# Optimization experiments

Measured on AMD Instinct MI355X. Metric: run time of the kernel, lower is better.

## Reference

```python
import jax, jax.numpy as jnp
import numpy as np
from jax import lax

B, C, DM, NL, NROI, HID, RHID, REMB = 2, 32, 64, 4, 90, 64, 64, 32
S = DM * DM * DM
EPS = 1e-5
DN = ('NCDHW', 'OIDHW', 'NCDHW')


def setup_inputs() -> dict:
    key = jax.random.key(0)
    ks = jax.random.split(key, 14)
    w = lambda k, shp, s=0.05: (jax.random.normal(k, shp, jnp.float32) * s)
    atlas = (jax.random.uniform(ks[1], (NROI, S)) < 0.1).astype(jnp.float32)
    return {
        'data': jax.random.normal(ks[0], (B, 1, DM, DM, DM), jnp.float32),
        'atlas_mask': atlas,
        'conv0_w': w(ks[2], (C, 1, 3, 3, 3), 0.2),
        'conv0_b': w(ks[3], (C,)),
        'convs_w': w(ks[4], (NL - 1, C, C, 3, 3, 3)),
        'convs_b': w(ks[5], (NL - 1, C)),
        'scale_w1': w(ks[6], (NROI, C, HID)),
        'scale_b1': w(ks[7], (NROI, HID)),
        'scale_w2': w(ks[8], (NROI, HID, C)),
        'scale_b2': w(ks[9], (NROI, C)),
        'proj_w1': w(ks[10], (NROI, C, RHID)),
        'proj_b1': w(ks[11], (NROI, RHID)),
        'proj_w2': w(ks[12], (NROI, RHID, REMB)),
        'proj_b2': w(ks[13], (NROI, REMB)),
    }


def _inorm(x):
    # InstanceNorm3d(affine=False): normalize per (batch, channel) over spatial dims
    m = jnp.mean(x, axis=(2, 3, 4), keepdims=True)
    v = jnp.var(x, axis=(2, 3, 4), keepdims=True)
    return (x - m) * lax.rsqrt(v + EPS)


def _conv(x, w, b):
    y = lax.conv_general_dilated(x, w, (1, 1, 1), 'SAME', dimension_numbers=DN)
    return y + b[None, :, None, None, None]


def reference(data, atlas_mask, conv0_w, conv0_b, convs_w, convs_b,
              scale_w1, scale_b1, scale_w2, scale_b2,
              proj_w1, proj_b1, proj_w2, proj_b2):
    x = jax.nn.relu(_inorm(_conv(data, conv0_w, conv0_b)))
    for i in range(NL - 1):  # fixed small layer loop
        x = jax.nn.relu(_inorm(_conv(x, convs_w[i], convs_b[i])))
    emb = x.reshape(B, C, S)                                  # (B,C,S)
    # (B,C,S) x (S,n_roi) -> (B,n_roi,C), normalized by ROI voxel count
    roi = jnp.einsum('bcs,rs->brc', emb, atlas_mask)
    roi = roi / atlas_mask.sum(axis=-1)[None, :, None]
    # per-ROI gated MLP experts, batched over the roi axis
    h = jax.nn.relu(jnp.einsum('brc,rch->brh', roi, scale_w1) + scale_b1[None])
    gate = jax.nn.sigmoid(jnp.einsum('brh,rhc->brc', h, scale_w2) + scale_b2[None])
    f = gate * roi
    p = jax.nn.relu(jnp.einsum('brc,rch->brh', f, proj_w1) + proj_b1[None])
    out = jnp.einsum('brh,rhe->bre', p, proj_w2) + proj_b2[None]
    return out  # (B, n_roi, roi_emb)
```

## Files before the change

kernel.cpp:

```cpp
#include <hip/hip_runtime.h>
#include <hip/hip_bf16.h>
#include <math.h>

#define S_TOT 262144
#define EPS_F 1e-5f
#define NPART 512
#define PL8   8008

typedef __attribute__((ext_vector_type(8))) short s16x8;
typedef __attribute__((ext_vector_type(4))) float f32x4;
typedef __attribute__((ext_vector_type(4))) unsigned u32x4;

__device__ __forceinline__ unsigned short f2bf(float f) {
    unsigned u = __builtin_bit_cast(unsigned, f);
    unsigned r = (u + 0x7FFFu + ((u >> 16) & 1u)) >> 16;
    return (unsigned short)r;
}
__device__ __forceinline__ float bf2f(unsigned short u) {
    return __builtin_bit_cast(float, ((unsigned)u) << 16);
}
__device__ __forceinline__ unsigned cvt_pk_bf16(float a, float b) {
    unsigned r;
    asm("v_cvt_pk_bf16_f32 %0, %1, %2" : "=v"(r) : "v"(a), "v"(b));
    return r;
}

__global__ __launch_bounds__(256)
void prep_w_k(const float* __restrict__ conv0_w, const float* __restrict__ convs_w,
              unsigned short* __restrict__ wpad, unsigned short* __restrict__ whp)
{
    int idx = blockIdx.x * 256 + threadIdx.x;
    if (idx < 2048) {
        int brow = idx >> 5, k = idx & 31;
        int cout = 2 * (brow & 15) + (brow >> 4);
        float wv = (k < 27) ? conv0_w[cout * 27 + k] : 0.f;
        unsigned short hi = f2bf(wv);
        unsigned short lo = f2bf(wv - bf2f(hi));
        wpad[brow * 32 + k]        = hi;
        wpad[1024 + brow * 32 + k] = lo;
        return;
    }
    int j = idx - 2048;
    if (j >= 3 * 27648) return;
    int layer = j / 27648 + 1;
    int rem   = j % 27648;
    int tap   = rem >> 10;
    int cout  = (rem >> 5) & 31;
    int cin   = rem & 31;
    float wv = convs_w[(((layer - 1) * 32 + cout) * 32 + cin) * 27 + tap];
    unsigned short hi = f2bf(wv);
    int brow = ((cout & 1) << 4) | (cout >> 1);
    whp[(size_t)(layer - 1) * 27648 + tap * 1024 + brow * 32 + cin] = hi;
}

__global__ __launch_bounds__(512, 2)
void conv0_k(const float* __restrict__ in, const unsigned short* __restrict__ w0,
             unsigned short* __restrict__ outb, float* __restrict__ raw_out)
{
    __shared__ unsigned short sc[1824];
    __shared__ float s_red[512];

    const int tid  = threadIdx.x;
    const int lane = tid & 63;
    const int wv   = tid >> 6;
    const int row  = lane & 15;
    const int g4   = lane >> 4;

    const int blk = blockIdx.x;
    const int b   = blk >> 8;
    const int t   = blk & 255;
    const int x0  = (t & 7) << 3;
    const int y0  = ((t >> 3) & 7) << 3;
    const int z0  = (t >> 6) << 4;

    for (int i = tid; i < 1800; i += 512) {
        int zz = i / 100, r2 = i - zz * 100, yy = r2 / 10, xx = r2 - yy * 10;
        int gz = z0 + zz - 1, gy = y0 + yy - 1, gx = x0 + xx - 1;
        float v = 0.f;
        if ((unsigned)gz < 64u && (unsigned)gy < 64u && (unsigned)gx < 64u)
            v = in[((size_t)b << 18) + (gz << 12) + (gy << 6) + gx];
        sc[i] = (unsigned short)cvt_pk_bf16(v, v);
    }
    __syncthreads();

    int dvox[8];
    #pragma unroll
    for (int j = 0; j < 8; ++j) {
        int tap = g4 * 8 + j;
        if (tap < 27) {
            int dz = tap / 9, r9 = tap - dz * 9, dy = r9 / 3, dx = r9 - dy * 3;
            dvox[j] = dz * 100 + dy * 10 + dx;
        } else dvox[j] = 0;
    }

    s16x8 wh0 = *(const s16x8*)(w0 + row * 32 + g4 * 8);
    s16x8 wh1 = *(const s16x8*)(w0 + (16 + row) * 32 + g4 * 8);
    s16x8 wl0 = *(const s16x8*)(w0 + 1024 + row * 32 + g4 * 8);
    s16x8 wl1 = *(const s16x8*)(w0 + 1024 + (16 + row) * 32 + g4 * 8);

    f32x4 acc[2][4][2] = {};
    #pragma unroll
    for (int pl = 0; pl < 2; ++pl) {
        #pragma unroll
        for (int f = 0; f < 4; ++f) {
            int vvx = f * 16 + row;
            int base = (2 * wv + pl) * 100 + (vvx >> 3) * 10 + (vvx & 7);
            s16x8 a;
            #pragma unroll
            for (int j = 0; j < 8; ++j) a[j] = (short)sc[base + dvox[j]];
            acc[pl][f][0] = __builtin_amdgcn_mfma_f32_16x16x32_bf16(a, wh0, acc[pl][f][0], 0, 0, 0);
            acc[pl][f][0] = __builtin_amdgcn_mfma_f32_16x16x32_bf16(a, wl0, acc[pl][f][0], 0, 0, 0);
            acc[pl][f][1] = __builtin_amdgcn_mfma_f32_16x16x32_bf16(a, wh1, acc[pl][f][1], 0, 0, 0);
            acc[pl][f][1] = __builtin_amdgcn_mfma_f32_16x16x32_bf16(a, wl1, acc[pl][f][1], 0, 0, 0);
        }
    }

    {
        float s0 = 0.f, ss0 = 0.f, s1 = 0.f, ss1 = 0.f;
        #pragma unroll
        for (int pl = 0; pl < 2; ++pl)
            #pragma unroll
            for (int f = 0; f < 4; ++f)
                #pragma unroll
                for (int q = 0; q < 4; ++q) {
                    float v0 = acc[pl][f][0][q], v1 = acc[pl][f][1][q];
                    s0 += v0; ss0 += v0 * v0; s1 += v1; ss1 += v1 * v1;
                }
        s0 += __shfl_xor(s0, 16); s0 += __shfl_xor(s0, 32);
        ss0 += __shfl_xor(ss0, 16); ss0 += __shfl_xor(ss0, 32);
        s1 += __shfl_xor(s1, 16); s1 += __shfl_xor(s1, 32);
        ss1 += __shfl_xor(ss1, 16); ss1 += __shfl_xor(ss1, 32);
        if (lane < 16) {
            s_red[(wv * 32 + 2 * row) * 2]         = s0;
            s_red[(wv * 32 + 2 * row) * 2 + 1]     = ss0;
            s_red[(wv * 32 + 2 * row + 1) * 2]     = s1;
            s_red[(wv * 32 + 2 * row + 1) * 2 + 1] = ss1;
        }
    }

    #pragma unroll
    for (int pl = 0; pl < 2; ++pl) {
        int zp = 2 * wv + pl;
        unsigned short* ob = outb
            + ((((size_t)b << 18) + ((size_t)(z0 + zp) << 12) + (y0 << 6) + x0) << 5)
            + (row << 1);
        #pragma unroll
        for (int f = 0; f < 4; ++f) {
            #pragma unroll
            for (int qq = 0; qq < 4; ++qq) {
                int u = g4 * 4 + qq;
                int yy = f * 2 + (u >> 3), xx = u & 7;
                unsigned pk = cvt_pk_bf16(acc[pl][f][0][qq], acc[pl][f][1][qq]);
                *(unsigned*)(ob + ((yy << 6) + xx) * 32) = pk;
            }
        }
    }

    __syncthreads();
    if (tid < 64) {
        int n = tid & 31, sel = tid >> 5;
        float tot = 0.f;
        #pragma unroll
        for (int w = 0; w < 8; ++w) tot += s_red[(w * 32 + n) * 2 + sel];
        atomicAdd(&raw_out[(b * 32 + n) * 2 + sel], tot);
    }
}

__global__ __launch_bounds__(512, 4)
void conv_slab_k(const unsigned short* __restrict__ in, const unsigned short* __restrict__ whp_l,
                 const float* __restrict__ raw_in, unsigned short* __restrict__ outb,
                 float* __restrict__ raw_out)
{
    __shared__ unsigned short tile[4 * PL8];
    __shared__ float s_red[512];

    const int tid  = threadIdx.x;
    const int lane = tid & 63;
    const int wv   = tid >> 6;
    const int row  = lane & 15;
    const int g4   = lane >> 4;
    const int g    = tid & 3;
    const int vox0 = tid >> 2;

    const int blk = blockIdx.x;
    const int b   = blk >> 9;
    const int t   = blk & 511;
    const int x0  = (t & 7) << 3;
    const int y0  = ((t >> 3) & 7) << 3;
    const int z0  = (t >> 6) << 3;

    {
        float rs[8], sh[8];
        #pragma unroll
        for (int j = 0; j < 8; ++j) {
            int c = b * 32 + g * 8 + j;
            float sm = raw_in[c * 2], sq = raw_in[c * 2 + 1];
            float mean = sm * (1.f / 262144.f);
            float var  = sq * (1.f / 262144.f) - mean * mean;
            float r = rsqrtf(var + EPS_F);
            rs[j] = r; sh[j] = -mean * r;
        }
        #pragma unroll 1
        for (int u = 0; u < 8; ++u) {
            int vox = vox0 + u * 128;
            if (vox >= 1000) break;
            int zz = vox / 100, r2 = vox - zz * 100, yy = r2 / 10, xx = r2 - yy * 10;
            int gz = z0 + zz - 1, gy = y0 + yy - 1, gx = x0 + xx - 1;
            u32x4 w = (u32x4)0;
            if ((unsigned)gz < 64u && (unsigned)gy < 64u && (unsigned)gx < 64u) {
                u32x4 rv = *(const u32x4*)(in
                    + ((((size_t)b << 18) + (gz << 12) + (gy << 6) + gx) << 5) + (g << 3));
                #pragma unroll
                for (int k = 0; k < 4; ++k) {
                    float ve = __builtin_bit_cast(float, rv[k] << 16);
                    float vo = __builtin_bit_cast(float, rv[k] & 0xFFFF0000u);
                    float ne = fmaxf(0.f, fmaf(ve, rs[2 * k],     sh[2 * k]));
                    float no = fmaxf(0.f, fmaf(vo, rs[2 * k + 1], sh[2 * k + 1]));
                    w[k] = cvt_pk_bf16(ne, no);
                }
            }
            *(u32x4*)&tile[g * PL8 + (vox << 3)] = w;
        }
    }
    __syncthreads();

    f32x4 acc[4][2] = {};
    {
        const unsigned short* aplane = &tile[g4 * PL8];
        int abase[4];
        #pragma unroll
        for (int f = 0; f < 4; ++f) {
            int vvx = f * 16 + row;
            abase[f] = ((wv * 100 + (vvx >> 3) * 10 + (vvx & 7)) << 3);
        }
        const unsigned short* wrow = whp_l + row * 32 + g4 * 8;

        s16x8 wh0 = *(const s16x8*)(wrow);
        s16x8 wh1 = *(const s16x8*)(wrow + 512);

        #pragma unroll 1
        for (int tap = 0; tap < 27; ++tap) {
            int ntap = (tap < 26) ? tap + 1 : 26;
            const unsigned short* wn = wrow + ntap * 1024;
            s16x8 nh0 = *(const s16x8*)(wn);
            s16x8 nh1 = *(const s16x8*)(wn + 512);

            int dz = tap / 9, r9 = tap - dz * 9, dy = r9 / 3, dx = r9 - dy * 3;
            int doff = ((dz * 100 + dy * 10 + dx) << 3);
            s16x8 a0 = *(const s16x8*)&aplane[abase[0] + doff];
            s16x8 a1 = *(const s16x8*)&aplane[abase[1] + doff];
            s16x8 a2 = *(const s16x8*)&aplane[abase[2] + doff];
            s16x8 a3 = *(const s16x8*)&aplane[abase[3] + doff];
            acc[0][0] = __builtin_amdgcn_mfma_f32_16x16x32_bf16(a0, wh0, acc[0][0], 0, 0, 0);
            acc[1][0] = __builtin_amdgcn_mfma_f32_16x16x32_bf16(a1, wh0, acc[1][0], 0, 0, 0);
            acc[2][0] = __builtin_amdgcn_mfma_f32_16x16x32_bf16(a2, wh0, acc[2][0], 0, 0, 0);
            acc[3][0] = __builtin_amdgcn_mfma_f32_16x16x32_bf16(a3, wh0, acc[3][0], 0, 0, 0);
            acc[0][1] = __builtin_amdgcn_mfma_f32_16x16x32_bf16(a0, wh1, acc[0][1], 0, 0, 0);
            acc[1][1] = __builtin_amdgcn_mfma_f32_16x16x32_bf16(a1, wh1, acc[1][1], 0, 0, 0);
            acc[2][1] = __builtin_amdgcn_mfma_f32_16x16x32_bf16(a2, wh1, acc[2][1], 0, 0, 0);
            acc[3][1] = __builtin_amdgcn_mfma_f32_16x16x32_bf16(a3, wh1, acc[3][1], 0, 0, 0);
            wh0 = nh0; wh1 = nh1;
        }
    }

    {
        float s0 = 0.f, ss0 = 0.f, s1 = 0.f, ss1 = 0.f;
        #pragma unroll
        for (int f = 0; f < 4; ++f)
            #pragma unroll
            for (int q = 0; q < 4; ++q) {
                float v0 = acc[f][0][q], v1 = acc[f][1][q];
                s0 += v0; ss0 += v0 * v0; s1 += v1; ss1 += v1 * v1;
            }
        s0 += __shfl_xor(s0, 16); s0 += __shfl_xor(s0, 32);
        ss0 += __shfl_xor(ss0, 16); ss0 += __shfl_xor(ss0, 32);
        s1 += __shfl_xor(s1, 16); s1 += __shfl_xor(s1, 32);
        ss1 += __shfl_xor(ss1, 16); ss1 += __shfl_xor(ss1, 32);
        if (lane < 16) {
            s_red[(wv * 32 + 2 * row) * 2]         = s0;
            s_red[(wv * 32 + 2 * row) * 2 + 1]     = ss0;
            s_red[(wv * 32 + 2 * row + 1) * 2]     = s1;
            s_red[(wv * 32 + 2 * row + 1) * 2 + 1] = ss1;
        }
    }

    {
        unsigned short* ob = outb
            + ((((size_t)b << 18) + ((size_t)(z0 + wv) << 12) + (y0 << 6) + x0) << 5)
            + (row << 1);
        #pragma unroll
        for (int f = 0; f < 4; ++f) {
            #pragma unroll
            for (int qq = 0; qq < 4; ++qq) {
                int u = g4 * 4 + qq;
                int yy = f * 2 + (u >> 3), xx = u & 7;
                unsigned pk = cvt_pk_bf16(acc[f][0][qq], acc[f][1][qq]);
                *(unsigned*)(ob + ((yy << 6) + xx) * 32) = pk;
            }
        }
    }

    __syncthreads();
    if (tid < 64) {
        int n = tid & 31, sel = tid >> 5;
        float tot = 0.f;
        #pragma unroll
        for (int w = 0; w < 8; ++w) tot += s_red[(w * 32 + n) * 2 + sel];
        atomicAdd(&raw_out[(b * 32 + n) * 2 + sel], tot);
    }
}

__global__ __launch_bounds__(256)
void pool_mfma_k(const unsigned short* __restrict__ emb, const float* __restrict__ raw3,
                 const float* __restrict__ mask, float* __restrict__ part,
                 float* __restrict__ cntp)
{
    __shared__ unsigned short Ald[64 * 136];
    __shared__ unsigned short Bld[96 * 136];
    __shared__ float s_ns[128];

    const int tid  = threadIdx.x;
    const int lane = tid & 63, wv = tid >> 6;
    const int row  = lane & 15, g4 = lane >> 4;

    if (tid < 64) {
        float sm = raw3[tid * 2], sq = raw3[tid * 2 + 1];
        float mean = sm * (1.f / 262144.f);
        float var  = sq * (1.f / 262144.f) - mean * mean;
        float r = rsqrtf(var + EPS_F);
        s_ns[tid]      = r;
        s_ns[64 + tid] = -mean * r;
    }

    f32x4 acc[6] = {};
    float csum[6] = {};

    for (int ch = 0; ch < 4; ++ch) {
        const int s0 = (blockIdx.x * 4 + ch) << 7;
        __syncthreads();
        for (int i = tid; i < 1024; i += 256) {
            int bb = i >> 9, v = (i >> 2) & 127, g = i & 3;
            u32x4 rv = *(const u32x4*)(emb + (((size_t)bb << 18) + (size_t)(s0 + v)) * 32 + (g << 3));
            #pragma unroll
            for (int k = 0; k < 4; ++k) {
                int bc = bb * 32 + (g << 3) + 2 * k;
                float ve = __builtin_bit_cast(float, rv[k] << 16);
                float vo = __builtin_bit_cast(float, rv[k] & 0xFFFF0000u);
                float ne = fmaxf(0.f, fmaf(ve, s_ns[bc],     s_ns[64 + bc]));
                float no = fmaxf(0.f, fmaf(vo, s_ns[bc + 1], s_ns[64 + bc + 1]));
                unsigned pk = cvt_pk_bf16(ne, no);
                Ald[bc * 136 + v]       = (unsigned short)pk;
                Ald[(bc + 1) * 136 + v] = (unsigned short)(pk >> 16);
            }
        }
        #pragma unroll
        for (int k = 0; k < 6; ++k) {
            int i = tid + k * 256;
            int r = i >> 4, bs = i & 15;
            s16x8 vec = (s16x8)0;
            if (r < 90) {
                const float* mp = mask + (size_t)r * S_TOT + s0 + bs * 8;
                float4 m0 = *(const float4*)mp;
                float4 m1 = *(const float4*)(mp + 4);
                vec[0] = (m0.x != 0.f) ? (short)0x3F80 : (short)0;
                vec[1] = (m0.y != 0.f) ? (short)0x3F80 : (short)0;
                vec[2] = (m0.z != 0.f) ? (short)0x3F80 : (short)0;
                vec[3] = (m0.w != 0.f) ? (short)0x3F80 : (short)0;
                vec[4] = (m1.x != 0.f) ? (short)0x3F80 : (short)0;
                vec[5] = (m1.y != 0.f) ? (short)0x3F80 : (short)0;
                vec[6] = (m1.z != 0.f) ? (short)0x3F80 : (short)0;
                vec[7] = (m1.w != 0.f) ? (short)0x3F80 : (short)0;
                csum[k] += m0.x + m0.y + m0.z + m0.w + m1.x + m1.y + m1.z + m1.w;
            }
            *(s16x8*)&Bld[r * 136 + bs * 8] = vec;
        }
        __syncthreads();
        #pragma unroll
        for (int kk = 0; kk < 4; ++kk) {
            s16x8 a = *(const s16x8*)&Ald[(wv * 16 + row) * 136 + kk * 32 + g4 * 8];
            #pragma unroll
            for (int j = 0; j < 6; ++j) {
                s16x8 bb = *(const s16x8*)&Bld[(j * 16 + row) * 136 + kk * 32 + g4 * 8];
                acc[j] = __builtin_amdgcn_mfma_f32_16x16x32_bf16(a, bb, acc[j], 0, 0, 0);
            }
        }
    }
    #pragma unroll
    for (int k = 0; k < 6; ++k) {
        float c = csum[k];
        c += __shfl_xor(c, 1); c += __shfl_xor(c, 2);
        c += __shfl_xor(c, 4); c += __shfl_xor(c, 8);
        if ((tid & 15) == 0)
            cntp[(size_t)blockIdx.x * 96 + (tid >> 4) + k * 16] = c;
    }
    #pragma unroll
    for (int j = 0; j < 6; ++j) {
        *(f32x4*)&part[((size_t)blockIdx.x * 96 + j * 16 + row) * 64 + wv * 16 + g4 * 4]
            = acc[j];
    }
}

__global__ __launch_bounds__(256)
void mlp_k(const float* __restrict__ part, const float* __restrict__ cntp,
           const float* __restrict__ w1, const float* __restrict__ b1,
           const float* __restrict__ w2, const float* __restrict__ b2,
           const float* __restrict__ pw1, const float* __restrict__ pb1,
           const float* __restrict__ pw2, const float* __restrict__ pb2,
           float* __restrict__ out)
{
    const int r   = blockIdx.x % 90;
    const int b   = blockIdx.x / 90;
    const int tid = threadIdx.x;
    __shared__ float sred[8 * 32];
    __shared__ float scnt[4];
    __shared__ float roi_s[32], h_s[64], f_s[32], p_s[64];

    {
        float csp = 0.f;
        for (int p = tid; p < NPART; p += 256) csp += cntp[(size_t)p * 96 + r];
        #pragma unroll
        for (int off = 32; off > 0; off >>= 1) csp += __shfl_xor(csp, off);
        if ((tid & 63) == 0) scnt[tid >> 6] = csp;
    }
    {
        const int c = tid & 31, seg = tid >> 5;
        const float* pp = part + ((size_t)(seg * (NPART / 8)) * 96 + r) * 64 + b * 32 + c;
        float s = 0.f;
        #pragma unroll 4
        for (int p = 0; p < NPART / 8; ++p) s += pp[(size_t)p * 6144];
        sred[seg * 32 + c] = s;
    }
    __syncthreads();
    if (tid < 32) {
        float cs = scnt[0] + scnt[1] + scnt[2] + scnt[3];
        float t = 0.f;
        #pragma unroll
        for (int k = 0; k < 8; ++k) t += sred[k * 32 + tid];
        roi_s[tid] = t / cs;
    }
    __syncthreads();
    if (tid < 64) {
        float s = b1[r * 64 + tid];
        for (int c = 0; c < 32; ++c)
            s = fmaf(roi_s[c], w1[(r * 32 + c) * 64 + tid], s);
        h_s[tid] = fmaxf(s, 0.f);
    }
    __syncthreads();
    if (tid < 32) {
        float s = b2[r * 32 + tid];
        for (int j = 0; j < 64; ++j)
            s = fmaf(h_s[j], w2[(r * 64 + j) * 32 + tid], s);
        float gate = 1.f / (1.f + expf(-s));
        f_s[tid] = gate * roi_s[tid];
    }
    __syncthreads();
    if (tid < 64) {
        float s = pb1[r * 64 + tid];
        for (int c = 0; c < 32; ++c)
            s = fmaf(f_s[c], pw1[(r * 32 + c) * 64 + tid], s);
        p_s[tid] = fmaxf(s, 0.f);
    }
    __syncthreads();
    if (tid < 32) {
        float s = pb2[r * 32 + tid];
        for (int j = 0; j < 64; ++j)
            s = fmaf(p_s[j], pw2[(r * 64 + j) * 32 + tid], s);
        out[((size_t)b * 90 + r) * 32 + tid] = s;
    }
}

extern "C" void kernel_launch(void* const* d_in, const int* in_sizes, int n_in,
                              void* d_out, int out_size, void* d_ws, size_t ws_size,
                              hipStream_t stream)
{
    const float* data    = (const float*)d_in[0];
    const float* mask    = (const float*)d_in[1];
    const float* conv0_w = (const float*)d_in[2];
    const float* convs_w = (const float*)d_in[4];
    const float* sw1 = (const float*)d_in[6];
    const float* sb1 = (const float*)d_in[7];
    const float* sw2 = (const float*)d_in[8];
    const float* sb2 = (const float*)d_in[9];
    const float* pw1 = (const float*)d_in[10];
    const float* pb1 = (const float*)d_in[11];
    const float* pw2 = (const float*)d_in[12];
    const float* pb2 = (const float*)d_in[13];
    float* out = (float*)d_out;

    float* ws = (float*)d_ws;
    unsigned short* bufA = (unsigned short*)ws;
    unsigned short* bufB = (unsigned short*)(ws + 8388608);
    unsigned short* wpad = (unsigned short*)(ws + 16777216);
    unsigned short* whp  = (unsigned short*)(ws + 16887808);
    float* raw   = ws + 16929280;
    float* part  = ws + 17825792;
    float* cntp  = part + 3145728;

    hipMemsetAsync(raw, 0, 512 * sizeof(float), stream);
    prep_w_k<<<332, 256, 0, stream>>>(conv0_w, convs_w, wpad, whp);

    conv0_k<<<512, 512, 0, stream>>>(data, wpad, bufA, raw);
    conv_slab_k<<<1024, 512, 0, stream>>>(bufA, whp, raw, bufB, raw + 128);
    conv_slab_k<<<1024, 512, 0, stream>>>(bufB, whp + 27648, raw + 128, bufA, raw + 256);
    conv_slab_k<<<1024, 512, 0, stream>>>(bufA, whp + 2 * 27648, raw + 256, bufB, raw + 384);

    pool_mfma_k<<<NPART, 256, 0, stream>>>(bufB, raw + 384, mask, part, cntp);

    mlp_k<<<180, 256, 0, stream>>>(part, cntp, sw1, sb1, sw2, sb2,
                                   pw1, pb1, pw2, pb2, out);
}
```

Before: 235.5 us.

## Enlarge conv slab tile to 16x8x8 voxels to improve halo reuse

Widens each conv_slab_k block's output tile from 8x8x8 to 16x8x8 voxels (x doubled), halving the block count. The staged halo tile grows from 10x10x10 to 18x10x10, which cuts the fraction of redundant halo loads and normalisation work per output voxel. Each wave now keeps 8 accumulator fragments instead of 4, and each fragment maps to one 16-voxel x-row, which simplifies the output store addressing. The cost is higher register and LDS use, so launch bounds drop to 2 blocks per CU, and there are fewer blocks to fill the GPU.

```diff
diff --git a/kernel.cpp b/kernel.cpp
--- a/kernel.cpp
+++ b/kernel.cpp
@@ -5,7 +5,7 @@
 #define S_TOT 262144
 #define EPS_F 1e-5f
 #define NPART 512
-#define PL8   8008
+#define PLSTR 14416
 
 typedef __attribute__((ext_vector_type(8))) short s16x8;
 typedef __attribute__((ext_vector_type(4))) float f32x4;
@@ -166,12 +166,12 @@
     }
 }
 
-__global__ __launch_bounds__(512, 4)
+__global__ __launch_bounds__(512, 2)
 void conv_slab_k(const unsigned short* __restrict__ in, const unsigned short* __restrict__ whp_l,
                  const float* __restrict__ raw_in, unsigned short* __restrict__ outb,
                  float* __restrict__ raw_out)
 {
-    __shared__ unsigned short tile[4 * PL8];
+    __shared__ unsigned short tile[4 * PLSTR];
     __shared__ float s_red[512];
 
     const int tid  = threadIdx.x;
@@ -183,11 +183,11 @@
     const int vox0 = tid >> 2;
 
     const int blk = blockIdx.x;
-    const int b   = blk >> 9;
-    const int t   = blk & 511;
-    const int x0  = (t & 7) << 3;
-    const int y0  = ((t >> 3) & 7) << 3;
-    const int z0  = (t >> 6) << 3;
+    const int b   = blk >> 8;
+    const int t   = blk & 255;
+    const int x0  = (t & 3) << 4;
+    const int y0  = ((t >> 2) & 7) << 3;
+    const int z0  = (t >> 5) << 3;
 
     {
         float rs[8], sh[8];
@@ -201,10 +201,10 @@
             rs[j] = r; sh[j] = -mean * r;
         }
         #pragma unroll 1
-        for (int u = 0; u < 8; ++u) {
+        for (int u = 0; u < 15; ++u) {
             int vox = vox0 + u * 128;
-            if (vox >= 1000) break;
-            int zz = vox / 100, r2 = vox - zz * 100, yy = r2 / 10, xx = r2 - yy * 10;
+            if (vox >= 1800) break;
+            int zz = vox / 180, r2 = vox - zz * 180, yy = r2 / 18, xx = r2 - yy * 18;
             int gz = z0 + zz - 1, gy = y0 + yy - 1, gx = x0 + xx - 1;
             u32x4 w = (u32x4)0;
             if ((unsigned)gz < 64u && (unsigned)gy < 64u && (unsigned)gx < 64u) {
@@ -219,20 +219,18 @@
                     w[k] = cvt_pk_bf16(ne, no);
                 }
             }
-            *(u32x4*)&tile[g * PL8 + (vox << 3)] = w;
-        }
-    }
-    __syncthreads();
-
-    f32x4 acc[4][2] = {};
-    {
-        const unsigned short* aplane = &tile[g4 * PL8];
-        int abase[4];
-        #pragma unroll
-        for (int f = 0; f < 4; ++f) {
-            int vvx = f * 16 + row;
-            abase[f] = ((wv * 100 + (vvx >> 3) * 10 + (vvx & 7)) << 3);
-        }
+            *(u32x4*)&tile[g * PLSTR + (vox << 3)] = w;
+        }
+    }
+    __syncthreads();
+
+    f32x4 acc[8][2] = {};
+    {
+        const unsigned short* aplane = &tile[g4 * PLSTR];
+        int abase[8];
+        #pragma unroll
+        for (int fr = 0; fr < 8; ++fr)
+            abase[fr] = ((wv * 180 + fr * 18 + row) << 3);
         const unsigned short* wrow = whp_l + row * 32 + g4 * 8;
 
         s16x8 wh0 = *(const s16x8*)(wrow);
@@ -246,19 +244,13 @@
             s16x8 nh1 = *(const s16x8*)(wn + 512);
 
             int dz = tap / 9, r9 = tap - dz * 9, dy = r9 / 3, dx = r9 - dy * 3;
-            int doff = ((dz * 100 + dy * 10 + dx) << 3);
-            s16x8 a0 = *(const s16x8*)&aplane[abase[0] + doff];
-            s16x8 a1 = *(const s16x8*)&aplane[abase[1] + doff];
-            s16x8 a2 = *(const s16x8*)&aplane[abase[2] + doff];
-            s16x8 a3 = *(const s16x8*)&aplane[abase[3] + doff];
-            acc[0][0] = __builtin_amdgcn_mfma_f32_16x16x32_bf16(a0, wh0, acc[0][0], 0, 0, 0);
-            acc[1][0] = __builtin_amdgcn_mfma_f32_16x16x32_bf16(a1, wh0, acc[1][0], 0, 0, 0);
-            acc[2][0] = __builtin_amdgcn_mfma_f32_16x16x32_bf16(a2, wh0, acc[2][0], 0, 0, 0);
-            acc[3][0] = __builtin_amdgcn_mfma_f32_16x16x32_bf16(a3, wh0, acc[3][0], 0, 0, 0);
-            acc[0][1] = __builtin_amdgcn_mfma_f32_16x16x32_bf16(a0, wh1, acc[0][1], 0, 0, 0);
-            acc[1][1] = __builtin_amdgcn_mfma_f32_16x16x32_bf16(a1, wh1, acc[1][1], 0, 0, 0);
-            acc[2][1] = __builtin_amdgcn_mfma_f32_16x16x32_bf16(a2, wh1, acc[2][1], 0, 0, 0);
-            acc[3][1] = __builtin_amdgcn_mfma_f32_16x16x32_bf16(a3, wh1, acc[3][1], 0, 0, 0);
+            int doff = ((dz * 180 + dy * 18 + dx) << 3);
+            #pragma unroll
+            for (int fr = 0; fr < 8; ++fr) {
+                s16x8 a = *(const s16x8*)&aplane[abase[fr] + doff];
+                acc[fr][0] = __builtin_amdgcn_mfma_f32_16x16x32_bf16(a, wh0, acc[fr][0], 0, 0, 0);
+                acc[fr][1] = __builtin_amdgcn_mfma_f32_16x16x32_bf16(a, wh1, acc[fr][1], 0, 0, 0);
+            }
             wh0 = nh0; wh1 = nh1;
         }
     }
@@ -266,10 +258,10 @@
     {
         float s0 = 0.f, ss0 = 0.f, s1 = 0.f, ss1 = 0.f;
         #pragma unroll
-        for (int f = 0; f < 4; ++f)
+        for (int fr = 0; fr < 8; ++fr)
             #pragma unroll
             for (int q = 0; q < 4; ++q) {
-                float v0 = acc[f][0][q], v1 = acc[f][1][q];
+                float v0 = acc[fr][0][q], v1 = acc[fr][1][q];
                 s0 += v0; ss0 += v0 * v0; s1 += v1; ss1 += v1 * v1;
             }
         s0 += __shfl_xor(s0, 16); s0 += __shfl_xor(s0, 32);
@@ -284,19 +276,15 @@
         }
     }
 
-    {
+    #pragma unroll
+    for (int fr = 0; fr < 8; ++fr) {
         unsigned short* ob = outb
-            + ((((size_t)b << 18) + ((size_t)(z0 + wv) << 12) + (y0 << 6) + x0) << 5)
+            + ((((size_t)b << 18) + ((size_t)(z0 + wv) << 12) + ((y0 + fr) << 6) + x0) << 5)
             + (row << 1);
         #pragma unroll
-        for (int f = 0; f < 4; ++f) {
-            #pragma unroll
-            for (int qq = 0; qq < 4; ++qq) {
-                int u = g4 * 4 + qq;
-                int yy = f * 2 + (u >> 3), xx = u & 7;
-                unsigned pk = cvt_pk_bf16(acc[f][0][qq], acc[f][1][qq]);
-                *(unsigned*)(ob + ((yy << 6) + xx) * 32) = pk;
-            }
+        for (int qq = 0; qq < 4; ++qq) {
+            unsigned pk = cvt_pk_bf16(acc[fr][0][qq], acc[fr][1][qq]);
+            *(unsigned*)(ob + ((g4 * 4 + qq) << 5)) = pk;
         }
     }
 
@@ -500,9 +488,9 @@
     prep_w_k<<<332, 256, 0, stream>>>(conv0_w, convs_w, wpad, whp);
 
     conv0_k<<<512, 512, 0, stream>>>(data, wpad, bufA, raw);
-    conv_slab_k<<<1024, 512, 0, stream>>>(bufA, whp, raw, bufB, raw + 128);
-    conv_slab_k<<<1024, 512, 0, stream>>>(bufB, whp + 27648, raw + 128, bufA, raw + 256);
-    conv_slab_k<<<1024, 512, 0, stream>>>(bufA, whp + 2 * 27648, raw + 256, bufB, raw + 384);
+    conv_slab_k<<<512, 512, 0, stream>>>(bufA, whp, raw, bufB, raw + 128);
+    conv_slab_k<<<512, 512, 0, stream>>>(bufB, whp + 27648, raw + 128, bufA, raw + 256);
+    conv_slab_k<<<512, 512, 0, stream>>>(bufA, whp + 2 * 27648, raw + 256, bufB, raw + 384);
 
     pool_mfma_k<<<NPART, 256, 0, stream>>>(bufB, raw + 384, mask, part, cntp);
 
```

New measurement: 224.6 us. 1.05x faster.
